# Performance work log

Hardware: AMD Instinct MI355X
Metric: run time of the kernel (lower is better)

The kernel has to match this reference:

```python
import jax, jax.numpy as jnp
import numpy as np


def _degree_norms(src, dst, n_nodes):
    ones = jnp.ones(src.shape[0], dtype=jnp.float32)
    deg_out = jax.ops.segment_sum(ones, src, num_segments=n_nodes)
    deg_in = jax.ops.segment_sum(ones, dst, num_segments=n_nodes)
    # DGL GraphConv clamps degrees to min 1 before pow(-0.5)
    norm_src = jnp.power(jnp.maximum(deg_out, 1.0), -0.5)
    norm_dst = jnp.power(jnp.maximum(deg_in, 1.0), -0.5)
    return norm_src, norm_dst


def _graph_conv(h, src, dst, norm_src, norm_dst, W, b, activation):
    n_nodes = h.shape[0]
    # norm='both': scale source features, project, aggregate, scale dest
    x = h * norm_src[:, None]
    x = x @ W                                   # [N, out]
    m = x[src]                                  # gather  [E, out]
    agg = jax.ops.segment_sum(m, dst, num_segments=n_nodes)  # scatter-add [N, out]
    out = agg * norm_dst[:, None] + b
    if activation is not None:
        out = activation(out)
    return out


def setup_inputs() -> dict:
    key = jax.random.key(0)
    k = jax.random.split(key, 6)
    N, E, F, D = 100000, 1600000, 128, 128
    feature = jax.random.normal(k[0], (N, F), dtype=jnp.float32)
    src = jax.random.randint(k[1], (E,), 0, N, dtype=jnp.int32)
    dst = jax.random.randint(k[2], (E,), 0, N, dtype=jnp.int32)
    W1 = jax.random.normal(k[3], (F, D), dtype=jnp.float32) / np.sqrt(F)
    b1 = jnp.zeros((D,), dtype=jnp.float32)
    W2 = jax.random.normal(k[4], (D, D), dtype=jnp.float32) / np.sqrt(D)
    b2 = jnp.zeros((D,), dtype=jnp.float32)
    return {"feature": feature, "src": src, "dst": dst,
            "W1": W1, "b1": b1, "W2": W2, "b2": b2}


def reference(feature, src, dst, W1, b1, W2, b2):
    n_nodes = feature.shape[0]
    norm_src, norm_dst = _degree_norms(src, dst, n_nodes)
    # layer 0: relu; layer 1 (last): no activation
    h = _graph_conv(feature, src, dst, norm_src, norm_dst, W1, b1, jax.nn.relu)
    h = _graph_conv(h, src, dst, norm_src, norm_dst, W2, b2, None)
    return h
```

## Files before the change

kernel.cpp:

```cpp
#include <hip/hip_runtime.h>


#define RS_LOG 10
#define RS (1 << RS_LOG)

typedef short bf16x8 __attribute__((ext_vector_type(8)));
typedef float f32x4 __attribute__((ext_vector_type(4)));

__device__ __forceinline__ unsigned short rne_bf16(float v) {
  unsigned u = __float_as_uint(v);
  return (unsigned short)((u + 0x7FFF + ((u >> 16) & 1)) >> 16);
}

__device__ __forceinline__ void load_lds16(const void* g, void* l) {
  __builtin_amdgcn_global_load_lds((const __attribute__((address_space(1))) unsigned*)g,
                                   (__attribute__((address_space(3))) unsigned*)l, 16, 0, 0);
}

__global__ void build_graph(const int* __restrict__ src, const int* __restrict__ dst,
                            int* __restrict__ cursor, int* __restrict__ deg_out,
                            int* __restrict__ padded, int E, int CAP) {
  int e = blockIdx.x * blockDim.x + threadIdx.x;
  if (e < E) {
    int s = src[e];
    int d = dst[e];
    atomicAdd(&deg_out[s], 1);
    int pos = atomicAdd(&cursor[d], 1);
    if (pos < CAP) padded[(size_t)d * CAP + pos] = s;
  }
}

__global__ __launch_bounds__(256) void partition_edges(
    const int* __restrict__ src, const int* __restrict__ dst, int* __restrict__ g_cnt,
    int* __restrict__ part_dst, unsigned short* __restrict__ part_src, int E, int NR, int CAPR,
    int EPB) {
  __shared__ int cntD[256], cntS[256], baseD[256], baseS[256];
  int t = threadIdx.x;
  int e0 = blockIdx.x * EPB;
  int e1 = min(e0 + EPB, E);
  for (int i = t; i < NR; i += 256) {
    cntD[i] = 0;
    cntS[i] = 0;
  }
  __syncthreads();
  for (int e = e0 + t; e < e1; e += 256) {
    atomicAdd(&cntD[dst[e] >> RS_LOG], 1);
    atomicAdd(&cntS[src[e] >> RS_LOG], 1);
  }
  __syncthreads();
  for (int i = t; i < NR; i += 256) {
    baseD[i] = atomicAdd(&g_cnt[i * 16], cntD[i]);
    baseS[i] = atomicAdd(&g_cnt[(NR + i) * 16], cntS[i]);
    cntD[i] = 0;
    cntS[i] = 0;
  }
  __syncthreads();
  for (int e = e0 + t; e < e1; e += 256) {
    int s = src[e];
    int d = dst[e];
    int rd = d >> RS_LOG;
    int rs = s >> RS_LOG;
    int pd = baseD[rd] + atomicAdd(&cntD[rd], 1);
    if (pd < CAPR) part_dst[(size_t)rd * CAPR + pd] = ((d & (RS - 1)) << 17) | s;
    int ps = baseS[rs] + atomicAdd(&cntS[rs], 1);
    if (ps < CAPR) part_src[(size_t)rs * CAPR + ps] = (unsigned short)(s & (RS - 1));
  }
}

__global__ __launch_bounds__(512) void build_structures(
    const int* __restrict__ g_cnt, const int* __restrict__ part_dst,
    const unsigned short* __restrict__ part_src, int* __restrict__ padded,
    int* __restrict__ deg_in, int* __restrict__ deg_out, int N, int NR, int CAPR, int CAP) {
  __shared__ int cur[RS];
  int t = threadIdx.x;
  int b = blockIdx.x;
  for (int i = t; i < RS; i += 512) cur[i] = 0;
  __syncthreads();
  if (b < NR) {
    int cnt = min(g_cnt[b * 16], CAPR);
    const int* p = part_dst + (size_t)b * CAPR;
    for (int i = t; i < cnt; i += 512) {
      int v = p[i];
      int dlow = v >> 17;
      int s = v & 0x1FFFF;
      int pos = atomicAdd(&cur[dlow], 1);
      if (pos < CAP) padded[((size_t)((b << RS_LOG) + dlow)) * CAP + pos] = s;
    }
    __syncthreads();
    int nbase = b << RS_LOG;
    for (int i = t; i < RS; i += 512) {
      int node = nbase + i;
      if (node < N) deg_in[node] = cur[i];
    }
  } else {
    int r = b - NR;
    int cnt = min(g_cnt[(NR + r) * 16], CAPR);
    const unsigned short* p = part_src + (size_t)r * CAPR;
    for (int i = t; i < cnt; i += 512) atomicAdd(&cur[p[i]], 1);
    __syncthreads();
    int nbase = r << RS_LOG;
    for (int i = t; i < RS; i += 512) {
      int node = nbase + i;
      if (node < N) deg_out[node] = cur[i];
    }
  }
}

__global__ void compute_norms(const int* __restrict__ deg_out, const int* __restrict__ deg_in,
                              float* __restrict__ norm_src, float* __restrict__ norm_dst, int N) {
  int i = blockIdx.x * blockDim.x + threadIdx.x;
  if (i < N) {
    norm_src[i] = rsqrtf((float)max(deg_out[i], 1));
    norm_dst[i] = rsqrtf((float)max(deg_in[i], 1));
  }
}

__global__ __launch_bounds__(256) void prep_w(const float* __restrict__ W,
                                              unsigned short* __restrict__ Wt_hi,
                                              unsigned short* __restrict__ Wt_lo) {
  int idx = blockIdx.x * 256 + threadIdx.x;
  int k = idx >> 7;
  int c = idx & 127;
  float w = W[idx];
  unsigned short h = rne_bf16(w);
  float hf = __uint_as_float((unsigned)h << 16);
  unsigned short l = rne_bf16(w - hf);
  Wt_hi[c * 128 + k] = h;
  Wt_lo[c * 128 + k] = l;
}

__global__ __launch_bounds__(256, 4) void gemm_mfma_lds(const float* __restrict__ X,
                                                        const unsigned short* __restrict__ Wt_hi,
                                                        const unsigned short* __restrict__ Wt_lo,
                                                        const float* __restrict__ norm,
                                                        unsigned short* __restrict__ Ybf, int N) {
  __shared__ unsigned char XlB[32768] __attribute__((aligned(128)));
  int t = threadIdx.x;
  int lane = t & 63;
  int wv = t >> 6;
  int l = lane;
  int tile_r0 = blockIdx.x * 64;
  long valid_bytes = ((long)N - tile_r0) * 512;

  const char* xbase = (const char*)X + (size_t)tile_r0 * 512;
#pragma unroll
  for (int j = 0; j < 8; j++) {
    int d = j * 4096 + wv * 1024 + l * 16;
    int off = d ^ (((d >> 9) & 7) << 4);
    if (off >= valid_bytes) off = 0;
    load_lds16(xbase + off, XlB + j * 4096 + wv * 1024);
  }
  asm volatile("s_waitcnt vmcnt(0)" ::: "memory");
  __syncthreads();

  int c = lane & 15;
  int kgrp = lane >> 4;
  int rowA = tile_r0 + wv * 16 + c;
  bool okA = rowA < N;
  float nn = okA ? norm[rowA] : 0.f;
  const unsigned short* pbh = Wt_hi + (size_t)c * 128;
  const unsigned short* pbl = Wt_lo + (size_t)c * 128;

  f32x4 acc[8];
#pragma unroll
  for (int nr = 0; nr < 8; nr++) acc[nr] = (f32x4){0.f, 0.f, 0.f, 0.f};

#pragma unroll
  for (int s = 0; s < 4; s++) {
    int kb = s * 32 + kgrp * 8;
    int rloc = wv * 16 + c;
    int byteA = rloc * 512 + kb * 4;
    int a0 = byteA ^ ((rloc & 7) << 4);
    float4 xa = *(const float4*)(XlB + a0);
    float4 xb = *(const float4*)(XlB + (a0 ^ 16));
    bf16x8 ah, al;
    {
      float v[8] = {xa.x, xa.y, xa.z, xa.w, xb.x, xb.y, xb.z, xb.w};
#pragma unroll
      for (int j = 0; j < 8; j++) {
        float a = v[j] * nn;
        unsigned short h = rne_bf16(a);
        ah[j] = (short)h;
        al[j] = (short)rne_bf16(a - __uint_as_float((unsigned)h << 16));
      }
    }
#pragma unroll
    for (int nr = 0; nr < 8; nr++) {
      bf16x8 bh = *(const bf16x8*)(pbh + nr * 2048 + kb);
      bf16x8 bl = *(const bf16x8*)(pbl + nr * 2048 + kb);
      acc[nr] = __builtin_amdgcn_mfma_f32_16x16x32_bf16(ah, bh, acc[nr], 0, 0, 0);
      acc[nr] = __builtin_amdgcn_mfma_f32_16x16x32_bf16(al, bh, acc[nr], 0, 0, 0);
      acc[nr] = __builtin_amdgcn_mfma_f32_16x16x32_bf16(ah, bl, acc[nr], 0, 0, 0);
    }
  }

  int rb = tile_r0 + wv * 16 + kgrp * 4;
#pragma unroll
  for (int q = 0; q < 4; q++) {
    int row = rb + q;
    if (row < N) {
      unsigned short* yo = Ybf + (size_t)row * 128 + c;
#pragma unroll
      for (int nr = 0; nr < 8; nr++) yo[nr * 16] = rne_bf16(acc[nr][q]);
    }
  }
}

__global__ __launch_bounds__(256) void spmm_bf(const unsigned* __restrict__ Ybf,
                                               const int* __restrict__ padded,
                                               const int* __restrict__ deg_in,
                                               const float* __restrict__ norm_dst,
                                               const float* __restrict__ bias,
                                               float* __restrict__ out, int N, int CAP,
                                               int do_relu) {
  int t = threadIdx.x;
  int lane = t & 63;
  int wv = t >> 6;
  int v = blockIdx.x * 4 + wv;
  if (v >= N) return;
  int cnt = min(deg_in[v], CAP);
  int sidx = (lane < cnt) ? padded[(size_t)v * CAP + lane] : 0;
  float ax = 0.f, ay = 0.f;
  int i = 0;
  for (; i + 4 <= cnt; i += 4) {
    int s0 = __builtin_amdgcn_readlane(sidx, i);
    int s1 = __builtin_amdgcn_readlane(sidx, i + 1);
    int s2 = __builtin_amdgcn_readlane(sidx, i + 2);
    int s3 = __builtin_amdgcn_readlane(sidx, i + 3);
    unsigned w0 = Ybf[(size_t)s0 * 64 + lane];
    unsigned w1 = Ybf[(size_t)s1 * 64 + lane];
    unsigned w2 = Ybf[(size_t)s2 * 64 + lane];
    unsigned w3 = Ybf[(size_t)s3 * 64 + lane];
    ax += __uint_as_float(w0 << 16) + __uint_as_float(w1 << 16) +
          __uint_as_float(w2 << 16) + __uint_as_float(w3 << 16);
    ay += __uint_as_float(w0 & 0xFFFF0000u) + __uint_as_float(w1 & 0xFFFF0000u) +
          __uint_as_float(w2 & 0xFFFF0000u) + __uint_as_float(w3 & 0xFFFF0000u);
  }
  for (; i < cnt; i++) {
    int s = __builtin_amdgcn_readlane(sidx, i);
    unsigned w = Ybf[(size_t)s * 64 + lane];
    ax += __uint_as_float(w << 16);
    ay += __uint_as_float(w & 0xFFFF0000u);
  }
  float nd = norm_dst[v];
  float2 b = ((const float2*)bias)[lane];
  float2 r;
  r.x = ax * nd + b.x;
  r.y = ay * nd + b.y;
  if (do_relu) {
    r.x = fmaxf(r.x, 0.f);
    r.y = fmaxf(r.y, 0.f);
  }
  ((float2*)out)[(size_t)v * 64 + lane] = r;
}

extern "C" void kernel_launch(void* const* d_in, const int* in_sizes, int n_in,
                              void* d_out, int out_size, void* d_ws, size_t ws_size,
                              hipStream_t stream) {
  const float* feature = (const float*)d_in[0];
  const int* src = (const int*)d_in[1];
  const int* dst = (const int*)d_in[2];
  const float* W1 = (const float*)d_in[3];
  const float* b1 = (const float*)d_in[4];
  const float* W2 = (const float*)d_in[5];
  const float* b2 = (const float*)d_in[6];
  float* out = (float*)d_out;

  const int F = 128;
  int N = in_sizes[0] / F;
  int E = in_sizes[1];
  (void)n_in;
  (void)out_size;

  char* ws = (char*)d_ws;
  size_t off = 0;
  auto alloc = [&](size_t bytes) -> char* {
    char* p = ws + off;
    off = (off + bytes + 255) & ~(size_t)255;
    return p;
  };
  float* h_buf = (float*)alloc((size_t)N * F * 4);
  int* degs = (int*)alloc((size_t)2 * N * 4);
  int* deg_in_ = degs;
  int* deg_out_ = degs + N;
  float* norm_src = (float*)alloc((size_t)N * 4);
  float* norm_dst = (float*)alloc((size_t)N * 4);
  unsigned short* wt1_hi = (unsigned short*)alloc(128 * 128 * 2);
  unsigned short* wt1_lo = (unsigned short*)alloc(128 * 128 * 2);
  unsigned short* wt2_hi = (unsigned short*)alloc(128 * 128 * 2);
  unsigned short* wt2_lo = (unsigned short*)alloc(128 * 128 * 2);

  int NR = (N + RS - 1) >> RS_LOG;
  int CAPR = (E + NR - 1) / NR + 4096;
  CAPR = (CAPR + 31) & ~31;
  size_t part_bytes =
      (size_t)NR * CAPR * 4 + (size_t)NR * CAPR * 2 + (size_t)2 * NR * 16 * 4 + 1024;
  size_t avail = (ws_size > off) ? ws_size - off : 0;

  int CAP;
  bool partition_ok = (N <= 131072) && (NR <= 256);
  bool use_part;
  if (partition_ok && avail >= (size_t)N * 64 * 4 + part_bytes) {
    CAP = 64;
    use_part = true;
  } else if (partition_ok && avail >= (size_t)N * 48 * 4 + part_bytes) {
    CAP = 48;
    use_part = true;
  } else if (avail >= (size_t)N * 64 * 4 + (size_t)N * 4 + 256) {
    CAP = 64;
    use_part = false;
  } else if (avail >= (size_t)N * 48 * 4 + (size_t)N * 4 + 256) {
    CAP = 48;
    use_part = false;
  } else {
    CAP = 32;
    use_part = false;
  }
  int* padded = (int*)alloc((size_t)N * CAP * 4);

  prep_w<<<64, 256, 0, stream>>>(W1, wt1_hi, wt1_lo);
  prep_w<<<64, 256, 0, stream>>>(W2, wt2_hi, wt2_lo);

  if (use_part) {
    int* part_dst = (int*)alloc((size_t)NR * CAPR * 4);
    unsigned short* part_src = (unsigned short*)alloc((size_t)NR * CAPR * 2);
    int* g_cnt = (int*)alloc((size_t)2 * NR * 16 * 4);
    const int EPB = 4096;
    int NB = (E + EPB - 1) / EPB;
    hipMemsetAsync(g_cnt, 0, (size_t)2 * NR * 16 * 4, stream);
    partition_edges<<<NB, 256, 0, stream>>>(src, dst, g_cnt, part_dst, part_src, E, NR, CAPR,
                                            EPB);
    build_structures<<<2 * NR, 512, 0, stream>>>(g_cnt, part_dst, part_src, padded, deg_in_,
                                                 deg_out_, N, NR, CAPR, CAP);
  } else {
    int* cursor = (int*)alloc((size_t)N * 4);
    hipMemsetAsync(degs, 0, (size_t)2 * N * 4, stream);
    build_graph<<<(E + 255) / 256, 256, 0, stream>>>(src, dst, deg_in_, deg_out_, padded, E, CAP);
    (void)cursor;
  }
  compute_norms<<<(N + 255) / 256, 256, 0, stream>>>(deg_out_, deg_in_, norm_src, norm_dst, N);

  unsigned short* ybf1 = (unsigned short*)d_out;
  unsigned short* ybf2;
  float* final_target;
  bool need_copy;
  size_t ybf_bytes = (size_t)N * 128 * 2;
  if (ws_size > off && ws_size - off >= ybf_bytes + 256) {
    ybf2 = (unsigned short*)alloc(ybf_bytes);
    final_target = out;
    need_copy = false;
  } else {
    ybf2 = (unsigned short*)d_out;
    final_target = h_buf;
    need_copy = true;
  }

  int gblocks = (N + 63) / 64;
  gemm_mfma_lds<<<gblocks, 256, 0, stream>>>(feature, wt1_hi, wt1_lo, norm_src, ybf1, N);
  spmm_bf<<<(N + 3) / 4, 256, 0, stream>>>((const unsigned*)ybf1, padded, deg_in_, norm_dst, b1,
                                           h_buf, N, CAP, 1);
  gemm_mfma_lds<<<gblocks, 256, 0, stream>>>(h_buf, wt2_hi, wt2_lo, norm_src, ybf2, N);
  spmm_bf<<<(N + 3) / 4, 256, 0, stream>>>((const unsigned*)ybf2, padded, deg_in_, norm_dst, b2,
                                           final_target, N, CAP, 0);
  if (need_copy) {
    hipMemcpyAsync(out, h_buf, (size_t)N * F * 4, hipMemcpyDeviceToDevice, stream);
  }
}
```

Before: 410.9 us.

## Persistent double-buffered GEMM with LDS-resident W fragments; stage partition writes in LDS

The GEMM becomes a persistent kernel with 256 blocks of 512 threads. Each block loads the pre-fragmented bf16 hi/lo weights into 64KB of LDS once, then double-buffers X tiles so the next tile's load overlaps the current tile's MFMAs. Edge partitioning now stages edges per block in LDS, sorted by range through a prefix scan, before writing them out, which should make global writes more coalesced. The costs are 128KB of dynamic LDS per block, which allows only one block per CU, and extra barriers and a scan in the partition kernel.

```diff
diff --git a/kernel.cpp b/kernel.cpp
--- a/kernel.cpp
+++ b/kernel.cpp
@@ -3,6 +3,7 @@
 
 #define RS_LOG 10
 #define RS (1 << RS_LOG)
+#define EPB 4096
 
 typedef short bf16x8 __attribute__((ext_vector_type(8)));
 typedef float f32x4 __attribute__((ext_vector_type(4)));
@@ -32,38 +33,67 @@
 
 __global__ __launch_bounds__(256) void partition_edges(
     const int* __restrict__ src, const int* __restrict__ dst, int* __restrict__ g_cnt,
-    int* __restrict__ part_dst, unsigned short* __restrict__ part_src, int E, int NR, int CAPR,
-    int EPB) {
-  __shared__ int cntD[256], cntS[256], baseD[256], baseS[256];
+    int* __restrict__ part_dst, unsigned short* __restrict__ part_src, int E, int NR, int CAPR) {
+  __shared__ int cntD[256], locD[256], baseD[256];
+  __shared__ int cntS[256], locS[256], baseS[256];
+  __shared__ unsigned stageD[EPB];
+  __shared__ unsigned short stageS[EPB];
+  __shared__ unsigned char rngD[EPB], rngS[EPB];
   int t = threadIdx.x;
   int e0 = blockIdx.x * EPB;
   int e1 = min(e0 + EPB, E);
-  for (int i = t; i < NR; i += 256) {
-    cntD[i] = 0;
-    cntS[i] = 0;
-  }
+  int nE = e1 - e0;
+  cntD[t] = 0;
+  cntS[t] = 0;
   __syncthreads();
   for (int e = e0 + t; e < e1; e += 256) {
     atomicAdd(&cntD[dst[e] >> RS_LOG], 1);
     atomicAdd(&cntS[src[e] >> RS_LOG], 1);
   }
   __syncthreads();
-  for (int i = t; i < NR; i += 256) {
-    baseD[i] = atomicAdd(&g_cnt[i * 16], cntD[i]);
-    baseS[i] = atomicAdd(&g_cnt[(NR + i) * 16], cntS[i]);
-    cntD[i] = 0;
-    cntS[i] = 0;
-  }
+  locD[t] = cntD[t];
+  locS[t] = cntS[t];
+  __syncthreads();
+  for (int ofs = 1; ofs < 256; ofs <<= 1) {
+    int aD = (t >= ofs) ? locD[t - ofs] : 0;
+    int aS = (t >= ofs) ? locS[t - ofs] : 0;
+    __syncthreads();
+    locD[t] += aD;
+    locS[t] += aS;
+    __syncthreads();
+  }
+  int exD = locD[t] - cntD[t];
+  int exS = locS[t] - cntS[t];
+  __syncthreads();
+  locD[t] = exD;
+  locS[t] = exS;
+  if (t < NR) {
+    baseD[t] = atomicAdd(&g_cnt[t * 16], cntD[t]);
+    baseS[t] = atomicAdd(&g_cnt[(NR + t) * 16], cntS[t]);
+  }
+  cntD[t] = 0;
+  cntS[t] = 0;
   __syncthreads();
   for (int e = e0 + t; e < e1; e += 256) {
     int s = src[e];
     int d = dst[e];
     int rd = d >> RS_LOG;
     int rs = s >> RS_LOG;
-    int pd = baseD[rd] + atomicAdd(&cntD[rd], 1);
-    if (pd < CAPR) part_dst[(size_t)rd * CAPR + pd] = ((d & (RS - 1)) << 17) | s;
-    int ps = baseS[rs] + atomicAdd(&cntS[rs], 1);
-    if (ps < CAPR) part_src[(size_t)rs * CAPR + ps] = (unsigned short)(s & (RS - 1));
+    int pd = locD[rd] + atomicAdd(&cntD[rd], 1);
+    stageD[pd] = ((unsigned)(d & (RS - 1)) << 17) | (unsigned)s;
+    rngD[pd] = (unsigned char)rd;
+    int ps = locS[rs] + atomicAdd(&cntS[rs], 1);
+    stageS[ps] = (unsigned short)(s & (RS - 1));
+    rngS[ps] = (unsigned char)rs;
+  }
+  __syncthreads();
+  for (int i = t; i < nE; i += 256) {
+    int r = rngD[i];
+    int pos = baseD[r] + (i - locD[r]);
+    if (pos < CAPR) part_dst[(size_t)r * CAPR + pos] = stageD[i];
+    int r2 = rngS[i];
+    int pos2 = baseS[r2] + (i - locS[r2]);
+    if (pos2 < CAPR) part_src[(size_t)r2 * CAPR + pos2] = stageS[i];
   }
 }
 
@@ -115,94 +145,123 @@
   }
 }
 
-__global__ __launch_bounds__(256) void prep_w(const float* __restrict__ W,
-                                              unsigned short* __restrict__ Wt_hi,
-                                              unsigned short* __restrict__ Wt_lo) {
+__global__ __launch_bounds__(256) void prep_w_frag(const float* __restrict__ W,
+                                                   unsigned short* __restrict__ Wfrag) {
   int idx = blockIdx.x * 256 + threadIdx.x;
-  int k = idx >> 7;
-  int c = idx & 127;
-  float w = W[idx];
+  int j = idx & 7;
+  int l = (idx >> 3) & 63;
+  int chunk = idx >> 9;
+  int nr = chunk >> 2;
+  int s = chunk & 3;
+  int col = nr * 16 + (l & 15);
+  int k = s * 32 + (l >> 4) * 8 + j;
+  float w = W[k * 128 + col];
   unsigned short h = rne_bf16(w);
   float hf = __uint_as_float((unsigned)h << 16);
-  unsigned short l = rne_bf16(w - hf);
-  Wt_hi[c * 128 + k] = h;
-  Wt_lo[c * 128 + k] = l;
-}
-
-__global__ __launch_bounds__(256, 4) void gemm_mfma_lds(const float* __restrict__ X,
-                                                        const unsigned short* __restrict__ Wt_hi,
-                                                        const unsigned short* __restrict__ Wt_lo,
-                                                        const float* __restrict__ norm,
-                                                        unsigned short* __restrict__ Ybf, int N) {
-  __shared__ unsigned char XlB[32768] __attribute__((aligned(128)));
+  unsigned short lo = rne_bf16(w - hf);
+  Wfrag[((chunk * 2 + 0) * 64 + l) * 8 + j] = h;
+  Wfrag[((chunk * 2 + 1) * 64 + l) * 8 + j] = lo;
+}
+
+__global__ __launch_bounds__(512, 1) void gemm_mfma_p(const float* __restrict__ X,
+                                                      const unsigned short* __restrict__ Wfrag,
+                                                      const float* __restrict__ norm,
+                                                      unsigned short* __restrict__ Ybf, int N) {
+  extern __shared__ unsigned char smem[];
+  unsigned char* Wl = smem;
+  unsigned char* Xa = smem + 65536;
+  unsigned char* Xb = smem + 98304;
   int t = threadIdx.x;
   int lane = t & 63;
   int wv = t >> 6;
-  int l = lane;
-  int tile_r0 = blockIdx.x * 64;
-  long valid_bytes = ((long)N - tile_r0) * 512;
-
-  const char* xbase = (const char*)X + (size_t)tile_r0 * 512;
+
 #pragma unroll
   for (int j = 0; j < 8; j++) {
-    int d = j * 4096 + wv * 1024 + l * 16;
-    int off = d ^ (((d >> 9) & 7) << 4);
-    if (off >= valid_bytes) off = 0;
-    load_lds16(xbase + off, XlB + j * 4096 + wv * 1024);
-  }
+    int d = j * 8192 + t * 16;
+    load_lds16((const unsigned char*)Wfrag + d, Wl + d);
+  }
+
+  auto stage = [&](unsigned char* dstb, int tr0) {
+    long vb = ((long)N - tr0) * 512;
+    const unsigned char* xbase = (const unsigned char*)X + (size_t)tr0 * 512;
+#pragma unroll
+    for (int j = 0; j < 4; j++) {
+      int d = j * 8192 + t * 16;
+      int off = d ^ (((d >> 9) & 7) << 4);
+      long o = off;
+      if (o >= vb) o = 0;
+      load_lds16(xbase + o, dstb + d);
+    }
+  };
+
+  int tile = blockIdx.x;
+  stage(Xa, tile * 64);
   asm volatile("s_waitcnt vmcnt(0)" ::: "memory");
   __syncthreads();
 
   int c = lane & 15;
   int kgrp = lane >> 4;
-  int rowA = tile_r0 + wv * 16 + c;
-  bool okA = rowA < N;
-  float nn = okA ? norm[rowA] : 0.f;
-  const unsigned short* pbh = Wt_hi + (size_t)c * 128;
-  const unsigned short* pbl = Wt_lo + (size_t)c * 128;
-
-  f32x4 acc[8];
-#pragma unroll
-  for (int nr = 0; nr < 8; nr++) acc[nr] = (f32x4){0.f, 0.f, 0.f, 0.f};
-
-#pragma unroll
-  for (int s = 0; s < 4; s++) {
-    int kb = s * 32 + kgrp * 8;
-    int rloc = wv * 16 + c;
-    int byteA = rloc * 512 + kb * 4;
-    int a0 = byteA ^ ((rloc & 7) << 4);
-    float4 xa = *(const float4*)(XlB + a0);
-    float4 xb = *(const float4*)(XlB + (a0 ^ 16));
-    bf16x8 ah, al;
-    {
-      float v[8] = {xa.x, xa.y, xa.z, xa.w, xb.x, xb.y, xb.z, xb.w};
-#pragma unroll
-      for (int j = 0; j < 8; j++) {
-        float a = v[j] * nn;
-        unsigned short h = rne_bf16(a);
-        ah[j] = (short)h;
-        al[j] = (short)rne_bf16(a - __uint_as_float((unsigned)h << 16));
+  int g = wv & 3;
+  int nb = (wv >> 2) * 4;
+  unsigned char* Xcur = Xa;
+  unsigned char* Xnxt = Xb;
+
+  for (; tile * 64 < N; tile += gridDim.x) {
+    int tr0 = tile * 64;
+    int nxt_r0 = (tile + gridDim.x) * 64;
+    if (nxt_r0 < N) stage(Xnxt, nxt_r0);
+
+    int rloc = g * 16 + c;
+    int rowA = tr0 + rloc;
+    float nn = (rowA < N) ? norm[rowA] : 0.f;
+    f32x4 acc[4];
+#pragma unroll
+    for (int nr = 0; nr < 4; nr++) acc[nr] = (f32x4){0.f, 0.f, 0.f, 0.f};
+
+#pragma unroll
+    for (int s = 0; s < 4; s++) {
+      int byteA = rloc * 512 + (s * 32 + kgrp * 8) * 4;
+      int a0 = byteA ^ ((rloc & 7) << 4);
+      float4 xa = *(const float4*)(Xcur + a0);
+      float4 xb2 = *(const float4*)(Xcur + (a0 ^ 16));
+      bf16x8 ah, al;
+      {
+        float v[8] = {xa.x, xa.y, xa.z, xa.w, xb2.x, xb2.y, xb2.z, xb2.w};
+#pragma unroll
+        for (int j = 0; j < 8; j++) {
+          float a = v[j] * nn;
+          unsigned short h = rne_bf16(a);
+          ah[j] = (short)h;
+          al[j] = (short)rne_bf16(a - __uint_as_float((unsigned)h << 16));
+        }
       }
-    }
-#pragma unroll
-    for (int nr = 0; nr < 8; nr++) {
-      bf16x8 bh = *(const bf16x8*)(pbh + nr * 2048 + kb);
-      bf16x8 bl = *(const bf16x8*)(pbl + nr * 2048 + kb);
-      acc[nr] = __builtin_amdgcn_mfma_f32_16x16x32_bf16(ah, bh, acc[nr], 0, 0, 0);
-      acc[nr] = __builtin_amdgcn_mfma_f32_16x16x32_bf16(al, bh, acc[nr], 0, 0, 0);
-      acc[nr] = __builtin_amdgcn_mfma_f32_16x16x32_bf16(ah, bl, acc[nr], 0, 0, 0);
-    }
-  }
-
-  int rb = tile_r0 + wv * 16 + kgrp * 4;
-#pragma unroll
-  for (int q = 0; q < 4; q++) {
-    int row = rb + q;
-    if (row < N) {
-      unsigned short* yo = Ybf + (size_t)row * 128 + c;
-#pragma unroll
-      for (int nr = 0; nr < 8; nr++) yo[nr * 16] = rne_bf16(acc[nr][q]);
-    }
+#pragma unroll
+      for (int nr = 0; nr < 4; nr++) {
+        int chunk = (nb + nr) * 4 + s;
+        bf16x8 bh = *(const bf16x8*)(Wl + (chunk * 2 + 0) * 1024 + lane * 16);
+        bf16x8 bl = *(const bf16x8*)(Wl + (chunk * 2 + 1) * 1024 + lane * 16);
+        acc[nr] = __builtin_amdgcn_mfma_f32_16x16x32_bf16(ah, bh, acc[nr], 0, 0, 0);
+        acc[nr] = __builtin_amdgcn_mfma_f32_16x16x32_bf16(al, bh, acc[nr], 0, 0, 0);
+        acc[nr] = __builtin_amdgcn_mfma_f32_16x16x32_bf16(ah, bl, acc[nr], 0, 0, 0);
+      }
+    }
+
+    asm volatile("s_waitcnt vmcnt(0)" ::: "memory");
+    __syncthreads();
+
+    int rb = tr0 + g * 16 + kgrp * 4;
+#pragma unroll
+    for (int q = 0; q < 4; q++) {
+      int row = rb + q;
+      if (row < N) {
+        unsigned short* yo = Ybf + (size_t)row * 128 + nb * 16 + c;
+#pragma unroll
+        for (int nr = 0; nr < 4; nr++) yo[nr * 16] = rne_bf16(acc[nr][q]);
+      }
+    }
+    unsigned char* tmp = Xcur;
+    Xcur = Xnxt;
+    Xnxt = tmp;
   }
 }
 
@@ -285,10 +344,8 @@
   int* deg_out_ = degs + N;
   float* norm_src = (float*)alloc((size_t)N * 4);
   float* norm_dst = (float*)alloc((size_t)N * 4);
-  unsigned short* wt1_hi = (unsigned short*)alloc(128 * 128 * 2);
-  unsigned short* wt1_lo = (unsigned short*)alloc(128 * 128 * 2);
-  unsigned short* wt2_hi = (unsigned short*)alloc(128 * 128 * 2);
-  unsigned short* wt2_lo = (unsigned short*)alloc(128 * 128 * 2);
+  unsigned short* wfrag1 = (unsigned short*)alloc(32768 * 2);
+  unsigned short* wfrag2 = (unsigned short*)alloc(32768 * 2);
 
   int NR = (N + RS - 1) >> RS_LOG;
   int CAPR = (E + NR - 1) / NR + 4096;
@@ -298,7 +355,7 @@
   size_t avail = (ws_size > off) ? ws_size - off : 0;
 
   int CAP;
-  bool partition_ok = (N <= 131072) && (NR <= 256);
+  bool partition_ok = (N <= 131072) && (NR <= 255);
   bool use_part;
   if (partition_ok && avail >= (size_t)N * 64 * 4 + part_bytes) {
     CAP = 64;
@@ -318,18 +375,16 @@
   }
   int* padded = (int*)alloc((size_t)N * CAP * 4);
 
-  prep_w<<<64, 256, 0, stream>>>(W1, wt1_hi, wt1_lo);
-  prep_w<<<64, 256, 0, stream>>>(W2, wt2_hi, wt2_lo);
+  prep_w_frag<<<64, 256, 0, stream>>>(W1, wfrag1);
+  prep_w_frag<<<64, 256, 0, stream>>>(W2, wfrag2);
 
   if (use_part) {
     int* part_dst = (int*)alloc((size_t)NR * CAPR * 4);
     unsigned short* part_src = (unsigned short*)alloc((size_t)NR * CAPR * 2);
     int* g_cnt = (int*)alloc((size_t)2 * NR * 16 * 4);
-    const int EPB = 4096;
     int NB = (E + EPB - 1) / EPB;
     hipMemsetAsync(g_cnt, 0, (size_t)2 * NR * 16 * 4, stream);
-    partition_edges<<<NB, 256, 0, stream>>>(src, dst, g_cnt, part_dst, part_src, E, NR, CAPR,
-                                            EPB);
+    partition_edges<<<NB, 256, 0, stream>>>(src, dst, g_cnt, part_dst, part_src, E, NR, CAPR);
     build_structures<<<2 * NR, 512, 0, stream>>>(g_cnt, part_dst, part_src, padded, deg_in_,
                                                  deg_out_, N, NR, CAPR, CAP);
   } else {
@@ -355,11 +410,12 @@
     need_copy = true;
   }
 
-  int gblocks = (N + 63) / 64;
-  gemm_mfma_lds<<<gblocks, 256, 0, stream>>>(feature, wt1_hi, wt1_lo, norm_src, ybf1, N);
+  int ntiles = (N + 63) / 64;
+  int gb = ntiles < 256 ? ntiles : 256;
+  gemm_mfma_p<<<gb, 512, 131072, stream>>>(feature, wfrag1, norm_src, ybf1, N);
   spmm_bf<<<(N + 3) / 4, 256, 0, stream>>>((const unsigned*)ybf1, padded, deg_in_, norm_dst, b1,
                                            h_buf, N, CAP, 1);
-  gemm_mfma_lds<<<gblocks, 256, 0, stream>>>(h_buf, wt2_hi, wt2_lo, norm_src, ybf2, N);
+  gemm_mfma_p<<<gb, 512, 131072, stream>>>(h_buf, wfrag2, norm_src, ybf2, N);
   spmm_bf<<<(N + 3) / 4, 256, 0, stream>>>((const unsigned*)ybf2, padded, deg_in_, norm_dst, b2,
                                            final_target, N, CAP, 0);
   if (need_copy) {
```

Result: faster. 333.6 us (-18.8%).
